# Kernel optimization log

Hardware: AMD Instinct MI355X
Metric: run time of the kernel (lower is better)

The kernel has to match this reference:

```python
import jax, jax.numpy as jnp
import numpy as np

B, S, D = 2, 2048, 2048
N_HEADS, N_KV_HEADS = 16, 4
HEAD_DIM = D // N_HEADS


def setup_inputs() -> dict:
    key = jax.random.key(0)
    ks = jax.random.split(key, 5)
    x = jax.random.normal(ks[0], (B, S, D), dtype=jnp.float32)
    W_q = jax.random.normal(ks[1], (D, D), dtype=jnp.float32) * 0.02
    W_k = jax.random.normal(ks[2], (D, N_KV_HEADS * HEAD_DIM), dtype=jnp.float32) * 0.02
    W_v = jax.random.normal(ks[3], (D, N_KV_HEADS * HEAD_DIM), dtype=jnp.float32) * 0.02
    W_o = jax.random.normal(ks[4], (D, D), dtype=jnp.float32) * 0.02
    return {"x": x, "W_q": W_q, "W_k": W_k, "W_v": W_v, "W_o": W_o}


def _apply_rope(xh, positions):
    # xh: [B, H, S, Dh]; rotate adjacent pairs as complex numbers
    Dh = xh.shape[-1]
    half = Dh // 2
    freqs = 1.0 / (10000.0 ** (jnp.arange(half, dtype=jnp.float32) / half))  # [half]
    angles = positions[:, None].astype(jnp.float32) * freqs[None, :]          # [S, half]
    cos, sin = jnp.cos(angles), jnp.sin(angles)
    xp = xh.reshape(*xh.shape[:-1], half, 2)
    x0, x1 = xp[..., 0], xp[..., 1]
    r0 = x0 * cos - x1 * sin
    r1 = x0 * sin + x1 * cos
    return jnp.stack([r0, r1], axis=-1).reshape(xh.shape)


def reference(x, W_q, W_k, W_v, W_o):
    b, s, d = x.shape
    positions = jnp.arange(s)
    rep = N_HEADS // N_KV_HEADS
    Q = (x @ W_q).reshape(b, s, N_HEADS, HEAD_DIM).transpose(0, 2, 1, 3)        # [B,H,S,Dh]
    K = (x @ W_k).reshape(b, s, N_KV_HEADS, HEAD_DIM).transpose(0, 2, 1, 3)     # [B,Hkv,S,Dh]
    V = (x @ W_v).reshape(b, s, N_KV_HEADS, HEAD_DIM).transpose(0, 2, 1, 3)
    Qr = _apply_rope(Q, positions)
    # torch .repeat(1, rep, 1, 1) tiles kv-head blocks: head h -> kv head h % n_kv_heads
    K_rep = jnp.tile(K, (1, rep, 1, 1))
    V_rep = jnp.tile(V, (1, rep, 1, 1))
    Kr = _apply_rope(K_rep, positions)
    scores = jnp.einsum('bhqd,bhkd->bhqk', Qr, Kr) / (HEAD_DIM ** 0.5)
    weights = jax.nn.softmax(scores, axis=-1)
    out = jnp.einsum('bhqk,bhkd->bhqd', weights, V_rep)
    out = out.transpose(0, 2, 1, 3).reshape(b, s, d)
    return out @ W_o
```

## Files before the change

kernel.cpp:

```cpp
#include <hip/hip_runtime.h>


typedef __attribute__((ext_vector_type(8))) short  short8;
typedef __attribute__((ext_vector_type(8))) __bf16 bf16x8;
typedef __attribute__((ext_vector_type(4))) float  f32x4;

#define B_   2
#define S_   2048
#define D_   2048
#define H_   16
#define HKV_ 4
#define DH_  128
#define M_   4096
#define NQKV 3072

static __device__ __forceinline__ ushort f2bf(float f) {
  __bf16 h = (__bf16)f;
  return __builtin_bit_cast(unsigned short, h);
}
static __device__ __forceinline__ float bf2f(ushort u) {
  union { unsigned u; float f; } v; v.u = ((unsigned)u) << 16;
  return v.f;
}
static __device__ __forceinline__ f32x4 mfma16(short8 a, short8 b, f32x4 c) {
  return __builtin_amdgcn_mfma_f32_16x16x32_bf16(
      __builtin_bit_cast(bf16x8, a), __builtin_bit_cast(bf16x8, b), c, 0, 0, 0);
}
static __device__ __forceinline__ void gload16(const ushort* g, ushort* l) {
  __builtin_amdgcn_global_load_lds(
      (const __attribute__((address_space(1))) unsigned int*)g,
      (__attribute__((address_space(3))) unsigned int*)l, 16, 0, 0);
}

__global__ void conv_f32_bf16(const float* __restrict__ in,
                              ushort* __restrict__ out, int n4) {
  int i = blockIdx.x * blockDim.x + threadIdx.x;
  if (i >= n4) return;
  float4 v = ((const float4*)in)[i];
  ushort4 o;
  o.x = f2bf(v.x); o.y = f2bf(v.y); o.z = f2bf(v.z); o.w = f2bf(v.w);
  ((ushort4*)out)[i] = o;
}

__global__ void transpose_conv(const float* __restrict__ in,
                               ushort* __restrict__ out, int R, int C) {
  __shared__ float tile[32][33];
  int c0 = blockIdx.x * 32, r0 = blockIdx.y * 32;
  int tx = threadIdx.x, ty = threadIdx.y;
#pragma unroll
  for (int i = 0; i < 32; i += 8)
    tile[ty + i][tx] = in[(size_t)(r0 + ty + i) * C + c0 + tx];
  __syncthreads();
#pragma unroll
  for (int i = 0; i < 32; i += 8)
    out[(size_t)(c0 + ty + i) * R + r0 + tx] = f2bf(tile[tx][ty + i]);
}

__global__ void transpose_v(const ushort* __restrict__ in,
                            ushort* __restrict__ out, int src_stride) {
  __shared__ ushort tile[32][33];
  int bkv = blockIdx.z;
  const ushort* src = in + (size_t)(bkv >> 2) * S_ * src_stride + (bkv & 3) * DH_;
  ushort* dst = out + (size_t)bkv * DH_ * S_;
  int d0 = blockIdx.x * 32, s0 = blockIdx.y * 32;
  int tx = threadIdx.x, ty = threadIdx.y;
#pragma unroll
  for (int i = 0; i < 32; i += 8)
    tile[ty + i][tx] = src[(size_t)(s0 + ty + i) * src_stride + d0 + tx];
  __syncthreads();
#pragma unroll
  for (int i = 0; i < 32; i += 8)
    dst[(size_t)(d0 + ty + i) * S_ + s0 + tx] = tile[tx][ty + i];
}

__global__ void rope_table_k(float2* __restrict__ tab) {
  int i = blockIdx.x * blockDim.x + threadIdx.x;
  int pos = i >> 6, f = i & 63;
  float freq = powf(10000.0f, -(float)f / 64.0f);
  float a = (float)pos * freq;
  tab[i] = make_float2(cosf(a), sinf(a));
}

__global__ void rope_apply_k(ushort* __restrict__ t,
                             const float2* __restrict__ tab,
                             int total, int ppr_shift, int row_stride,
                             float oscale) {
  int idx = blockIdx.x * blockDim.x + threadIdx.x;
  if (idx >= total) return;
  int row = idx >> ppr_shift;
  int p   = idx & ((1 << ppr_shift) - 1);
  int head = p >> 6, fi = p & 63;
  int pos = row & (S_ - 1);
  float2 cs = tab[(pos << 6) + fi];
  size_t off = (size_t)row * row_stride + head * DH_ + 2 * fi;
  ushort2 v = *(ushort2*)&t[off];
  float x0 = bf2f(v.x), x1 = bf2f(v.y);
  ushort2 o;
  o.x = f2bf((x0 * cs.x - x1 * cs.y) * oscale);
  o.y = f2bf((x0 * cs.y + x1 * cs.x) * oscale);
  *(ushort2*)&t[off] = o;
}

template <typename OutT>
__global__ __launch_bounds__(256) void gemm_bt(const ushort* __restrict__ A,
                                               const ushort* __restrict__ Bt,
                                               OutT* __restrict__ C,
                                               int M, int N, int K) {
  __shared__ ushort As[128 * 32];
  __shared__ ushort Bs[128 * 32];
  const int tid = threadIdx.x;
  const int lane = tid & 63, wave = tid >> 6;
  const int wm = (wave >> 1) * 64, wn = (wave & 1) * 64;
  const int bm = blockIdx.x * 128, bn = blockIdx.y * 128;
  const int l16 = lane & 15, l4 = lane >> 4;

  const ushort* gA = A  + (size_t)(bm + (tid >> 2)) * K + (tid & 3) * 8;
  const ushort* gB = Bt + (size_t)(bn + (tid >> 2)) * K + (tid & 3) * 8;
  ushort* lA0 = &As[wave * 512];
  ushort* lA1 = &As[2048 + wave * 512];
  ushort* lB0 = &Bs[wave * 512];
  ushort* lB1 = &Bs[2048 + wave * 512];
  const size_t rstep = (size_t)64 * K;

  f32x4 acc[4][4] = {};

  for (int k0 = 0; k0 < K; k0 += 32) {
    __syncthreads();
    gload16(gA + k0,         lA0);
    gload16(gA + k0 + rstep, lA1);
    gload16(gB + k0,         lB0);
    gload16(gB + k0 + rstep, lB1);
    __syncthreads();
    short8 af[4], bfr[4];
#pragma unroll
    for (int m = 0; m < 4; ++m)
      af[m] = *(const short8*)&As[(wm + m * 16 + l16) * 32 + l4 * 8];
#pragma unroll
    for (int n = 0; n < 4; ++n)
      bfr[n] = *(const short8*)&Bs[(wn + n * 16 + l16) * 32 + l4 * 8];
#pragma unroll
    for (int m = 0; m < 4; ++m)
#pragma unroll
      for (int n = 0; n < 4; ++n)
        acc[m][n] = mfma16(af[m], bfr[n], acc[m][n]);
  }

#pragma unroll
  for (int m = 0; m < 4; ++m) {
#pragma unroll
    for (int n = 0; n < 4; ++n) {
#pragma unroll
      for (int r = 0; r < 4; ++r) {
        size_t row = bm + wm + m * 16 + l4 * 4 + r;
        size_t col = bn + wn + n * 16 + l16;
        if constexpr (sizeof(OutT) == 2)
          C[row * N + col] = f2bf(acc[m][n][r]);
        else
          C[row * N + col] = acc[m][n][r];
      }
    }
  }
}

__global__ __launch_bounds__(256, 2) void flash_attn(const ushort* __restrict__ Qp,
                                                     const ushort* __restrict__ Kp,
                                                     const ushort* __restrict__ Vt,
                                                     ushort* __restrict__ Oa) {
  __shared__ ushort Ks[2][64 * 128];
  __shared__ ushort Vs[2][128 * 64];
  const int tid = threadIdx.x;
  const int lane = tid & 63, wave = tid >> 6;
  const int l16 = lane & 15, l4 = lane >> 4;
  const int bh = blockIdx.y;
  const int b = bh >> 4, h = bh & 15, kv = h & 3;
  const int q0 = blockIdx.x * 128 + wave * 32;

  short8 qf[2][4];
#pragma unroll
  for (int qg = 0; qg < 2; ++qg) {
    const ushort* qrow =
        Qp + ((size_t)(b * S_ + q0 + qg * 16 + l16)) * NQKV + h * DH_ + l4 * 8;
#pragma unroll
    for (int kk = 0; kk < 4; ++kk) qf[qg][kk] = *(const short8*)(qrow + kk * 32);
  }

  const ushort* kbase = Kp + (size_t)(b * S_) * NQKV + kv * DH_;
  const ushort* vbase = Vt + (size_t)(b * HKV_ + kv) * DH_ * S_;

  float mreg[2] = {-1e30f, -1e30f}, lsum[2] = {0.f, 0.f};
  f32x4 o[2][8] = {};

  const int kswz = (l16 & 3) | (((l16 >> 2) & 1) << 2);
  const int vswz = l16 & 7;

  const int krT = wave * 16 + (lane >> 4);
  const int kcT = lane & 15;
  const int vrT = wave * 32 + (lane >> 3);
  const int vcT = lane & 7;

  auto stage = [&](int t, int buf) {
#pragma unroll
    for (int i = 0; i < 4; ++i) {
      int r = krT + i * 4;
      int swz = (r & 3) | (((r >> 3) & 1) << 2);
      gload16(kbase + (size_t)(t * 64 + r) * NQKV + ((kcT ^ swz) * 8),
              &Ks[buf][(wave * 16 + i * 4) * 128]);
      int d = vrT + i * 8;
      gload16(vbase + (size_t)d * S_ + t * 64 + ((vcT ^ (d & 7)) * 8),
              &Vs[buf][(wave * 32 + i * 8) * 64]);
    }
  };

  const int NT = S_ / 64;
  stage(0, 0);
  __syncthreads();

  for (int t = 0; t < NT; ++t) {
    const int cur = t & 1;
    if (t + 1 < NT) stage(t + 1, cur ^ 1);

    f32x4 s[2][4] = {};
    __builtin_amdgcn_s_setprio(1);
#pragma unroll
    for (int c = 0; c < 4; ++c) {
      const int krow = 32 * (c >> 1) + 8 * (l16 >> 2) + 4 * (c & 1) + (l16 & 3);
#pragma unroll
      for (int kk = 0; kk < 4; ++kk) {
        short8 kf = *(const short8*)&Ks[cur][krow * 128 + (((kk * 4 + l4) ^ kswz) * 8)];
        s[0][c] = mfma16(kf, qf[0][kk], s[0][c]);
        s[1][c] = mfma16(kf, qf[1][kk], s[1][c]);
      }
    }
    __builtin_amdgcn_s_setprio(0);

    float tmax[2];
#pragma unroll
    for (int qg = 0; qg < 2; ++qg) {
      float a = fmaxf(fmaxf(s[qg][0][0], s[qg][0][1]), fmaxf(s[qg][0][2], s[qg][0][3]));
#pragma unroll
      for (int c = 1; c < 4; ++c) {
        a = fmaxf(a, fmaxf(fmaxf(s[qg][c][0], s[qg][c][1]),
                           fmaxf(s[qg][c][2], s[qg][c][3])));
      }
      a = fmaxf(a, __shfl_xor(a, 16));
      tmax[qg] = fmaxf(a, __shfl_xor(a, 32));
    }

    bool ok = (tmax[0] - mreg[0] <= 8.0f) && (tmax[1] - mreg[1] <= 8.0f);
    if (!__all(ok)) {
#pragma unroll
      for (int qg = 0; qg < 2; ++qg) {
        float mn = fmaxf(mreg[qg], tmax[qg]);
        float alpha = __builtin_amdgcn_exp2f(mreg[qg] - mn);
        mreg[qg] = mn;
        lsum[qg] *= alpha;
        float af[4];
#pragma unroll
        for (int r = 0; r < 4; ++r)
          af[r] = __shfl(alpha, (lane & 48) + l4 * 4 + r);
#pragma unroll
        for (int g = 0; g < 8; ++g)
#pragma unroll
          for (int r = 0; r < 4; ++r) o[qg][g][r] *= af[r];
      }
    }

    short8 pa[2][2];
    float rs[2] = {0.f, 0.f};
#pragma unroll
    for (int qg = 0; qg < 2; ++qg) {
#pragma unroll
      for (int ks = 0; ks < 2; ++ks) {
        short8 pk;
#pragma unroll
        for (int j = 0; j < 8; ++j) {
          float p = __builtin_amdgcn_exp2f(s[qg][2 * ks + (j >> 2)][j & 3] - mreg[qg]);
          rs[qg] += p;
          pk[j] = (short)f2bf(p);
        }
        pa[qg][ks] = pk;
      }
      float r2 = rs[qg] + __shfl_xor(rs[qg], 16);
      lsum[qg] += r2 + __shfl_xor(r2, 32);
    }

    __builtin_amdgcn_s_setprio(1);
#pragma unroll
    for (int ks = 0; ks < 2; ++ks) {
#pragma unroll
      for (int g = 0; g < 8; ++g) {
        const int d = g * 16 + l16;
        short8 vf = *(const short8*)&Vs[cur][d * 64 + (((ks * 4 + l4) ^ vswz) * 8)];
        o[0][g] = mfma16(pa[0][ks], vf, o[0][g]);
        o[1][g] = mfma16(pa[1][ks], vf, o[1][g]);
      }
    }
    __builtin_amdgcn_s_setprio(0);

    __syncthreads();
  }

#pragma unroll
  for (int qg = 0; qg < 2; ++qg) {
    float inv = 1.0f / lsum[qg];
    float invq[4];
#pragma unroll
    for (int r = 0; r < 4; ++r)
      invq[r] = __shfl(inv, (lane & 48) + l4 * 4 + r);
    ushort* op = Oa + (size_t)(b * S_ + q0 + qg * 16) * D_ + h * DH_;
#pragma unroll
    for (int g = 0; g < 8; ++g)
#pragma unroll
      for (int r = 0; r < 4; ++r)
        op[(size_t)(l4 * 4 + r) * D_ + g * 16 + l16] = f2bf(o[qg][g][r] * invq[r]);
  }
}

extern "C" void kernel_launch(void* const* d_in, const int* in_sizes, int n_in,
                              void* d_out, int out_size, void* d_ws, size_t ws_size,
                              hipStream_t stream) {
  (void)in_sizes; (void)n_in; (void)out_size; (void)ws_size;
  const float* x  = (const float*)d_in[0];
  const float* Wq = (const float*)d_in[1];
  const float* Wk = (const float*)d_in[2];
  const float* Wv = (const float*)d_in[3];
  const float* Wo = (const float*)d_in[4];
  float* out = (float*)d_out;

  size_t off = 0;
  auto carve = [&](size_t bytes) -> void* {
    void* p = (char*)d_ws + off;
    off += (bytes + 255) & ~(size_t)255;
    return p;
  };
  ushort* xb    = (ushort*)carve((size_t)M_ * D_ * 2);
  ushort* Wqkvt = (ushort*)carve((size_t)NQKV * D_ * 2);
  ushort* Wot   = (ushort*)carve((size_t)D_ * D_ * 2);
  ushort* QKV   = (ushort*)carve((size_t)M_ * NQKV * 2);
  ushort* Vt    = (ushort*)carve((size_t)M_ * 512 * 2);
  ushort* attn  = (ushort*)carve((size_t)M_ * D_ * 2);
  float2* tab   = (float2*)carve((size_t)S_ * 64 * sizeof(float2));

  conv_f32_bf16<<<(M_ * D_ / 4 + 255) / 256, 256, 0, stream>>>(x, xb, M_ * D_ / 4);
  transpose_conv<<<dim3(64, 64), dim3(32, 8), 0, stream>>>(Wq, Wqkvt, 2048, 2048);
  transpose_conv<<<dim3(16, 64), dim3(32, 8), 0, stream>>>(Wk, Wqkvt + (size_t)2048 * 2048, 2048, 512);
  transpose_conv<<<dim3(16, 64), dim3(32, 8), 0, stream>>>(Wv, Wqkvt + (size_t)2560 * 2048, 2048, 512);
  transpose_conv<<<dim3(64, 64), dim3(32, 8), 0, stream>>>(Wo, Wot, 2048, 2048);
  rope_table_k<<<(S_ * 64) / 256, 256, 0, stream>>>(tab);

  gemm_bt<ushort><<<dim3(32, 24), 256, 0, stream>>>(xb, Wqkvt, QKV, M_, NQKV, 2048);

  const float qscale = 0.08838834764831845f * 1.4426950408889634f;
  rope_apply_k<<<(M_ * 1024) / 256, 256, 0, stream>>>(QKV, tab, M_ * 1024, 10, NQKV, qscale);
  rope_apply_k<<<(M_ * 256) / 256, 256, 0, stream>>>(QKV + 2048, tab, M_ * 256, 8, NQKV, 1.0f);
  transpose_v<<<dim3(4, 64, 8), dim3(32, 8), 0, stream>>>(QKV + 2560, Vt, NQKV);

  flash_attn<<<dim3(S_ / 128, B_ * H_), 256, 0, stream>>>(QKV, QKV + 2048, Vt, attn);

  gemm_bt<float><<<dim3(32, 16), 256, 0, stream>>>(attn, Wot, out, M_, 2048, 2048);
}
```

Baseline: 242.3 us.

## Replace GEMM with 256-row tiled, triple-buffered, XOR-swizzled pipelined kernel

Replaces the 128x128 single-buffered GEMM with a 512-thread kernel using 256xBN tiles (BN=192 for QKV, 128 for output). It adds a three-stage LDS ring with async global-to-LDS loads issued two tiles ahead, explicit vmcnt waits, s_setprio around MFMA bursts, and an XOR swizzle on LDS columns to cut bank conflicts. The goal is to hide global load latency and raise data reuse per tile. In exchange it uses more LDS and registers and relies on hand-tuned waitcnt counts, which are fragile.

```diff
diff --git a/kernel.cpp b/kernel.cpp
--- a/kernel.cpp
+++ b/kernel.cpp
@@ -30,6 +30,10 @@
   __builtin_amdgcn_global_load_lds(
       (const __attribute__((address_space(1))) unsigned int*)g,
       (__attribute__((address_space(3))) unsigned int*)l, 16, 0, 0);
+}
+template <int N>
+static __device__ __forceinline__ void vmwait() {
+  asm volatile("s_waitcnt vmcnt(%0)" :: "n"(N) : "memory");
 }
 
 __global__ void conv_f32_bf16(const float* __restrict__ in,
@@ -101,62 +105,115 @@
   *(ushort2*)&t[off] = o;
 }
 
-template <typename OutT>
-__global__ __launch_bounds__(256) void gemm_bt(const ushort* __restrict__ A,
-                                               const ushort* __restrict__ Bt,
-                                               OutT* __restrict__ C,
-                                               int M, int N, int K) {
-  __shared__ ushort As[128 * 32];
-  __shared__ ushort Bs[128 * 32];
+template <int BN, int NF, typename OutT>
+__global__ __launch_bounds__(512, 2) void gemm256(const ushort* __restrict__ A,
+                                                  const ushort* __restrict__ Bt,
+                                                  OutT* __restrict__ C,
+                                                  int M, int N, int K) {
+  __shared__ ushort As[3][256 * 32];
+  __shared__ ushort Bs[3][BN * 32];
   const int tid = threadIdx.x;
-  const int lane = tid & 63, wave = tid >> 6;
-  const int wm = (wave >> 1) * 64, wn = (wave & 1) * 64;
-  const int bm = blockIdx.x * 128, bn = blockIdx.y * 128;
+  const int lane = tid & 63, w = tid >> 6;
   const int l16 = lane & 15, l4 = lane >> 4;
-
-  const ushort* gA = A  + (size_t)(bm + (tid >> 2)) * K + (tid & 3) * 8;
-  const ushort* gB = Bt + (size_t)(bn + (tid >> 2)) * K + (tid & 3) * 8;
-  ushort* lA0 = &As[wave * 512];
-  ushort* lA1 = &As[2048 + wave * 512];
-  ushort* lB0 = &Bs[wave * 512];
-  ushort* lB1 = &Bs[2048 + wave * 512];
-  const size_t rstep = (size_t)64 * K;
-
-  f32x4 acc[4][4] = {};
-
-  for (int k0 = 0; k0 < K; k0 += 32) {
-    __syncthreads();
-    gload16(gA + k0,         lA0);
-    gload16(gA + k0 + rstep, lA1);
-    gload16(gB + k0,         lB0);
-    gload16(gB + k0 + rstep, lB1);
-    __syncthreads();
-    short8 af[4], bfr[4];
-#pragma unroll
-    for (int m = 0; m < 4; ++m)
-      af[m] = *(const short8*)&As[(wm + m * 16 + l16) * 32 + l4 * 8];
-#pragma unroll
-    for (int n = 0; n < 4; ++n)
-      bfr[n] = *(const short8*)&Bs[(wn + n * 16 + l16) * 32 + l4 * 8];
-#pragma unroll
-    for (int m = 0; m < 4; ++m)
-#pragma unroll
-      for (int n = 0; n < 4; ++n)
-        acc[m][n] = mfma16(af[m], bfr[n], acc[m][n]);
+  const int wm = (w >> 2) * 128, wn = (w & 3) * (BN / 4);
+  const int bm = blockIdx.x * 256, bn = blockIdx.y * BN;
+
+  const ushort* gA = A  + (size_t)bm * K;
+  const ushort* gB = Bt + (size_t)bn * K;
+  const int srow = tid >> 2;
+  const int scol = (tid & 3) * 8;
+
+  constexpr int CT_HI = 2 + ((BN > 128) ? 2 : 1);
+  constexpr int CT_LO = 3;
+
+  auto stage = [&](int t, int s) {
+#pragma unroll
+    for (int j = 0; j < 2; ++j) {
+      int row = j * 128 + srow;
+      gload16(gA + (size_t)row * K + t * 32 + (scol ^ ((row & 3) << 3)),
+              &As[s][(j * 128 + w * 16) * 32]);
+    }
+    {
+      int row = srow;
+      gload16(gB + (size_t)row * K + t * 32 + (scol ^ ((row & 3) << 3)),
+              &Bs[s][(w * 16) * 32]);
+    }
+    if constexpr (BN > 128) {
+      if (tid < 256) {
+        int row = 128 + srow;
+        gload16(gB + (size_t)row * K + t * 32 + (scol ^ ((row & 3) << 3)),
+                &Bs[s][(128 + w * 16) * 32]);
+      }
+    }
+  };
+
+  f32x4 acc[8][NF] = {};
+  const int NT = K / 32;
+
+  stage(0, 0);
+  stage(1, 1);
+  if (BN > 128 && w < 4) vmwait<CT_HI>(); else vmwait<CT_LO>();
+  __builtin_amdgcn_s_barrier();
+  __builtin_amdgcn_sched_barrier(0);
+
+  for (int t = 0; t < NT; ++t) {
+    const int s = t - (t / 3) * 3;
+    if (t + 2 < NT) {
+      int s2 = (t + 2) - ((t + 2) / 3) * 3;
+      stage(t + 2, s2);
+    }
+    short8 bfr[NF];
+#pragma unroll
+    for (int ph = 0; ph < 2; ++ph) {
+      short8 afr[4];
+#pragma unroll
+      for (int mf = 0; mf < 4; ++mf) {
+        int row = wm + ph * 64 + mf * 16 + l16;
+        int col = l4 * 8;
+        afr[mf] = *(const short8*)&As[s][row * 32 + (col ^ ((row & 3) << 3))];
+      }
+      if (ph == 0) {
+#pragma unroll
+        for (int nf = 0; nf < NF; ++nf) {
+          int row = wn + nf * 16 + l16;
+          int col = l4 * 8;
+          bfr[nf] = *(const short8*)&Bs[s][row * 32 + (col ^ ((row & 3) << 3))];
+        }
+      }
+      __builtin_amdgcn_s_barrier();
+      asm volatile("s_waitcnt lgkmcnt(0)" ::: "memory");
+      __builtin_amdgcn_sched_barrier(0);
+      __builtin_amdgcn_s_setprio(1);
+#pragma unroll
+      for (int mf = 0; mf < 4; ++mf)
+#pragma unroll
+        for (int nf = 0; nf < NF; ++nf)
+          acc[ph * 4 + mf][nf] = mfma16(afr[mf], bfr[nf], acc[ph * 4 + mf][nf]);
+      __builtin_amdgcn_s_setprio(0);
+      if (ph == 1) {
+        if (t + 2 < NT) {
+          if (BN > 128 && w < 4) vmwait<CT_HI>(); else vmwait<CT_LO>();
+        } else if (t + 1 < NT) {
+          vmwait<0>();
+        }
+      }
+      __builtin_amdgcn_s_barrier();
+      __builtin_amdgcn_sched_barrier(0);
+    }
   }
 
 #pragma unroll
-  for (int m = 0; m < 4; ++m) {
-#pragma unroll
-    for (int n = 0; n < 4; ++n) {
+  for (int mi = 0; mi < 8; ++mi) {
+#pragma unroll
+    for (int nf = 0; nf < NF; ++nf) {
 #pragma unroll
       for (int r = 0; r < 4; ++r) {
-        size_t row = bm + wm + m * 16 + l4 * 4 + r;
-        size_t col = bn + wn + n * 16 + l16;
+        size_t row = bm + wm + (mi >> 2) * 64 + (mi & 3) * 16 + l4 * 4 + r;
+        size_t col = bn + wn + nf * 16 + l16;
         if constexpr (sizeof(OutT) == 2)
-          C[row * N + col] = f2bf(acc[m][n][r]);
+          C[row * N + col] = f2bf(acc[mi][nf][r]);
         else
-          C[row * N + col] = acc[m][n][r];
+          C[row * N + col] = acc[mi][nf][r];
       }
     }
   }
@@ -348,7 +405,7 @@
   transpose_conv<<<dim3(64, 64), dim3(32, 8), 0, stream>>>(Wo, Wot, 2048, 2048);
   rope_table_k<<<(S_ * 64) / 256, 256, 0, stream>>>(tab);
 
-  gemm_bt<ushort><<<dim3(32, 24), 256, 0, stream>>>(xb, Wqkvt, QKV, M_, NQKV, 2048);
+  gemm256<192, 3, ushort><<<dim3(16, 16), 512, 0, stream>>>(xb, Wqkvt, QKV, M_, NQKV, 2048);
 
   const float qscale = 0.08838834764831845f * 1.4426950408889634f;
   rope_apply_k<<<(M_ * 1024) / 256, 256, 0, stream>>>(QKV, tab, M_ * 1024, 10, NQKV, qscale);
@@ -357,5 +414,5 @@
 
   flash_attn<<<dim3(S_ / 128, B_ * H_), 256, 0, stream>>>(QKV, QKV + 2048, Vt, attn);
 
-  gemm_bt<float><<<dim3(32, 16), 256, 0, stream>>>(attn, Wot, out, M_, 2048, 2048);
-}
+  gemm256<128, 2, float><<<dim3(16, 16), 512, 0, stream>>>(attn, Wot, out, M_, 2048, 2048);
+}
```

After: 271.4 us. 1.12x slower.

## Replace GEMM with 512-thread double-buffered 8-phase pipelined kernel

Applied to the files above, without the earlier changes.

Replaces the simple 128x128 single-buffer GEMM with a 256xBN tile kernel using 8 waves, double-buffered LDS, XOR-swizzled layout and an 8-phase schedule that interleaves global-to-LDS loads with MFMA work, using explicit vmcnt waits and barriers. It targets the exposed load latency and the two full syncthreads per K-step of the old kernel, and increases data reuse per block. In exchange it needs larger LDS and register use at one block per CU, and its correctness depends on the hand-tuned wait counts.

```diff
diff --git a/kernel.cpp b/kernel.cpp
--- a/kernel.cpp
+++ b/kernel.cpp
@@ -30,6 +30,10 @@
   __builtin_amdgcn_global_load_lds(
       (const __attribute__((address_space(1))) unsigned int*)g,
       (__attribute__((address_space(3))) unsigned int*)l, 16, 0, 0);
+}
+template <int N>
+static __device__ __forceinline__ void vmwait() {
+  asm volatile("s_waitcnt vmcnt(%0)" :: "n"(N) : "memory");
 }
 
 __global__ void conv_f32_bf16(const float* __restrict__ in,
@@ -101,62 +105,130 @@
   *(ushort2*)&t[off] = o;
 }
 
-template <typename OutT>
-__global__ __launch_bounds__(256) void gemm_bt(const ushort* __restrict__ A,
-                                               const ushort* __restrict__ Bt,
-                                               OutT* __restrict__ C,
-                                               int M, int N, int K) {
-  __shared__ ushort As[128 * 32];
-  __shared__ ushort Bs[128 * 32];
+template <int BN, int NF, typename OutT>
+__global__ __launch_bounds__(512, 1) void gemm8p(const ushort* __restrict__ A,
+                                                 const ushort* __restrict__ Bt,
+                                                 OutT* __restrict__ C,
+                                                 int M, int N, int K) {
+  __shared__ ushort As[2][256 * 64];
+  __shared__ ushort Bs[2][BN * 64];
   const int tid = threadIdx.x;
-  const int lane = tid & 63, wave = tid >> 6;
-  const int wm = (wave >> 1) * 64, wn = (wave & 1) * 64;
-  const int bm = blockIdx.x * 128, bn = blockIdx.y * 128;
+  const int lane = tid & 63, w = tid >> 6;
   const int l16 = lane & 15, l4 = lane >> 4;
-
-  const ushort* gA = A  + (size_t)(bm + (tid >> 2)) * K + (tid & 3) * 8;
-  const ushort* gB = Bt + (size_t)(bn + (tid >> 2)) * K + (tid & 3) * 8;
-  ushort* lA0 = &As[wave * 512];
-  ushort* lA1 = &As[2048 + wave * 512];
-  ushort* lB0 = &Bs[wave * 512];
-  ushort* lB1 = &Bs[2048 + wave * 512];
-  const size_t rstep = (size_t)64 * K;
-
-  f32x4 acc[4][4] = {};
-
-  for (int k0 = 0; k0 < K; k0 += 32) {
-    __syncthreads();
-    gload16(gA + k0,         lA0);
-    gload16(gA + k0 + rstep, lA1);
-    gload16(gB + k0,         lB0);
-    gload16(gB + k0 + rstep, lB1);
-    __syncthreads();
-    short8 af[4], bfr[4];
-#pragma unroll
-    for (int m = 0; m < 4; ++m)
-      af[m] = *(const short8*)&As[(wm + m * 16 + l16) * 32 + l4 * 8];
-#pragma unroll
-    for (int n = 0; n < 4; ++n)
-      bfr[n] = *(const short8*)&Bs[(wn + n * 16 + l16) * 32 + l4 * 8];
-#pragma unroll
-    for (int m = 0; m < 4; ++m)
-#pragma unroll
-      for (int n = 0; n < 4; ++n)
-        acc[m][n] = mfma16(af[m], bfr[n], acc[m][n]);
-  }
-
-#pragma unroll
-  for (int m = 0; m < 4; ++m) {
-#pragma unroll
-    for (int n = 0; n < 4; ++n) {
+  const int wm = (w >> 2) * 128, wn = (w & 3) * (BN / 4);
+  const int bm = blockIdx.x * 256, bn = blockIdx.y * BN;
+  const int swz = l16 & 7;
+
+  const ushort* gA = A  + (size_t)bm * K;
+  const ushort* gB = Bt + (size_t)bn * K;
+  const int srow = tid >> 3;
+  const int scb  = tid & 7;
+  const int sswz = srow & 7;
+
+  auto stageA = [&](int t, int s, int g) {
+    int row = g * 64 + srow;
+    gload16(gA + (size_t)row * K + t * 64 + ((scb ^ sswz) * 8),
+            &As[s][(g * 64 + w * 8) * 64]);
+  };
+  auto stageB = [&](int t, int s, int g) {
+    int row = g * 64 + srow;
+    gload16(gB + (size_t)row * K + t * 64 + ((scb ^ sswz) * 8),
+            &Bs[s][(g * 64 + w * 8) * 64]);
+  };
+  auto stageB2 = [&](int t, int s) {
+    if constexpr (NF == 3) stageB(t, s, 2);
+  };
+
+  constexpr int VM_A = (NF == 3) ? 9 : 8;
+  constexpr int VM_B = (NF == 3) ? 7 : 6;
+
+  f32x4 acc[8][NF] = {};
+  short8 bfr[NF][2];
+  const int NT  = K / 64;
+  const int NIT = K / 128;
+
+  stageB(0, 0, 0); stageB(0, 0, 1); stageB2(0, 0);
+  stageA(0, 0, 0); stageA(0, 0, 2);
+  stageA(0, 0, 1); stageA(0, 0, 3);
+  stageB(1, 1, 0); stageB(1, 1, 1); stageB2(1, 1);
+  stageA(1, 1, 0); stageA(1, 1, 2);
+  vmwait<VM_B>();
+  __builtin_amdgcn_s_barrier();
+  __builtin_amdgcn_sched_barrier(0);
+
+#define GPHASE(S, J, ISSUES, VMW)                                             \
+  {                                                                           \
+    short8 afr[2][2];                                                         \
+    _Pragma("unroll")                                                         \
+    for (int mf = 0; mf < 2; ++mf) {                                          \
+      _Pragma("unroll")                                                       \
+      for (int kk = 0; kk < 2; ++kk) {                                        \
+        int row = wm + (J) * 32 + mf * 16 + l16;                              \
+        afr[mf][kk] =                                                         \
+            *(const short8*)&As[S][row * 64 + (((kk * 4 + l4) ^ swz) * 8)];   \
+      }                                                                       \
+    }                                                                         \
+    if ((J) == 0) {                                                           \
+      _Pragma("unroll")                                                       \
+      for (int nf = 0; nf < NF; ++nf) {                                       \
+        _Pragma("unroll")                                                     \
+        for (int kk = 0; kk < 2; ++kk) {                                      \
+          int row = wn + nf * 16 + l16;                                       \
+          bfr[nf][kk] =                                                       \
+              *(const short8*)&Bs[S][row * 64 + (((kk * 4 + l4) ^ swz) * 8)]; \
+        }                                                                     \
+      }                                                                       \
+    }                                                                         \
+    ISSUES;                                                                   \
+    __builtin_amdgcn_s_barrier();                                             \
+    asm volatile("s_waitcnt lgkmcnt(0)" ::: "memory");                        \
+    __builtin_amdgcn_sched_barrier(0);                                        \
+    __builtin_amdgcn_s_setprio(1);                                            \
+    _Pragma("unroll")                                                         \
+    for (int kk = 0; kk < 2; ++kk) {                                          \
+      _Pragma("unroll")                                                       \
+      for (int mf = 0; mf < 2; ++mf) {                                        \
+        _Pragma("unroll")                                                     \
+        for (int nf = 0; nf < NF; ++nf)                                       \
+          acc[(J) * 2 + mf][nf] =                                             \
+              mfma16(afr[mf][kk], bfr[nf][kk], acc[(J) * 2 + mf][nf]);        \
+      }                                                                       \
+    }                                                                         \
+    __builtin_amdgcn_s_setprio(0);                                            \
+    VMW;                                                                      \
+    __builtin_amdgcn_s_barrier();                                             \
+    __builtin_amdgcn_sched_barrier(0);                                        \
+  }
+
+  for (int i = 0; i < NIT; ++i) {
+    const int tb  = 2 * i + 1;
+    const int ta2 = (2 * i + 2 < NT) ? 2 * i + 2 : NT - 1;
+    const int tb2 = (2 * i + 3 < NT) ? 2 * i + 3 : NT - 1;
+    GPHASE(0, 0, (stageA(tb, 1, 1), stageA(tb, 1, 3)), (void)0)
+    GPHASE(0, 1, (stageB(ta2, 0, 0), stageB(ta2, 0, 1)), vmwait<VM_A>())
+    GPHASE(0, 2, (stageB2(ta2, 0), stageA(ta2, 0, 0)), (void)0)
+    GPHASE(0, 3, (stageA(ta2, 0, 2)), vmwait<VM_B>())
+    GPHASE(1, 0, (stageA(ta2, 0, 1), stageA(ta2, 0, 3)), (void)0)
+    GPHASE(1, 1, (stageB(tb2, 1, 0), stageB(tb2, 1, 1)), vmwait<VM_A>())
+    GPHASE(1, 2, (stageB2(tb2, 1), stageA(tb2, 1, 0)), (void)0)
+    GPHASE(1, 3, (stageA(tb2, 1, 2)), vmwait<VM_B>())
+  }
+#undef GPHASE
+
+  asm volatile("s_waitcnt vmcnt(0)" ::: "memory");
+
+#pragma unroll
+  for (int mi = 0; mi < 8; ++mi) {
+#pragma unroll
+    for (int nf = 0; nf < NF; ++nf) {
 #pragma unroll
       for (int r = 0; r < 4; ++r) {
-        size_t row = bm + wm + m * 16 + l4 * 4 + r;
-        size_t col = bn + wn + n * 16 + l16;
+        size_t row = bm + wm + (mi >> 1) * 32 + (mi & 1) * 16 + l4 * 4 + r;
+        size_t col = bn + wn + nf * 16 + l16;
         if constexpr (sizeof(OutT) == 2)
-          C[row * N + col] = f2bf(acc[m][n][r]);
+          C[row * N + col] = f2bf(acc[mi][nf][r]);
         else
-          C[row * N + col] = acc[m][n][r];
+          C[row * N + col] = acc[mi][nf][r];
       }
     }
   }
@@ -202,8 +274,8 @@
 #pragma unroll
     for (int i = 0; i < 4; ++i) {
       int r = krT + i * 4;
-      int swz = (r & 3) | (((r >> 3) & 1) << 2);
-      gload16(kbase + (size_t)(t * 64 + r) * NQKV + ((kcT ^ swz) * 8),
+      int swzk = (r & 3) | (((r >> 3) & 1) << 2);
+      gload16(kbase + (size_t)(t * 64 + r) * NQKV + ((kcT ^ swzk) * 8),
               &Ks[buf][(wave * 16 + i * 4) * 128]);
       int d = vrT + i * 8;
       gload16(vbase + (size_t)d * S_ + t * 64 + ((vcT ^ (d & 7)) * 8),
@@ -348,7 +420,7 @@
   transpose_conv<<<dim3(64, 64), dim3(32, 8), 0, stream>>>(Wo, Wot, 2048, 2048);
   rope_table_k<<<(S_ * 64) / 256, 256, 0, stream>>>(tab);
 
-  gemm_bt<ushort><<<dim3(32, 24), 256, 0, stream>>>(xb, Wqkvt, QKV, M_, NQKV, 2048);
+  gemm8p<192, 3, ushort><<<dim3(16, 16), 512, 0, stream>>>(xb, Wqkvt, QKV, M_, NQKV, 2048);
 
   const float qscale = 0.08838834764831845f * 1.4426950408889634f;
   rope_apply_k<<<(M_ * 1024) / 256, 256, 0, stream>>>(QKV, tab, M_ * 1024, 10, NQKV, qscale);
@@ -357,5 +429,5 @@
 
   flash_attn<<<dim3(S_ / 128, B_ * H_), 256, 0, stream>>>(QKV, QKV + 2048, Vt, attn);
 
-  gemm_bt<float><<<dim3(32, 16), 256, 0, stream>>>(attn, Wot, out, M_, 2048, 2048);
-}
+  gemm8p<128, 2, float><<<dim3(16, 16), 512, 0, stream>>>(attn, Wot, out, M_, 2048, 2048);
+}
```

After: 219.5 us. 9.4% less time.
